# Optimization experiments

Hardware: AMD Instinct MI355X
Metric: run time of the kernel (lower is better)

## Reference

```python
import jax, jax.numpy as jnp
import numpy as np

M = 2          # n_mix
D_K = 128      # feature dim
TEMP = float(np.sqrt(D_K))  # temperature = d_k ** 0.5


def setup_inputs() -> dict:
    key = jax.random.key(0)
    k1, k2, k3, k4 = jax.random.split(key, 4)
    BS, N, N2 = 8, 2048, 2048
    qt = jax.random.normal(k1, (BS, N, D_K), jnp.float32)
    kt = jax.random.normal(k2, (BS, N2, D_K), jnp.float32)
    vt = jax.random.normal(k3, (BS, N2, D_K), jnp.float32)
    std = M ** -0.5
    kernel = jax.random.uniform(k4, (M, D_K), jnp.float32, -std, std)
    return {"qt": qt, "kt": kt, "vt": vt, "kernel": kernel}


def reference(qt, kt, vt, kernel):
    # channels_last path of MixtureOfSoftMaxACF.call, training=False (dropout = identity)
    BS, N, dk = qt.shape
    N2 = kt.shape[1]
    d = dk // M
    # mixture prior: softmax(kernel @ mean_q^T) over axis=1 (faithful to Softmax(axis=1))
    bar_qt = jnp.mean(qt, axis=1)                       # (BS, dk)
    prior_mix = jax.nn.softmax(kernel @ bar_qt.T, axis=1)  # (m, BS)
    prior_mix = prior_mix.reshape(BS * M, 1, 1)            # row-major reshape, as in TF
    # split features into mixtures via row-major reshape (as tf.reshape does)
    q = qt.reshape(BS * M, N, d)
    k = kt.reshape(BS * M, N2, d)
    att = jnp.einsum('bnd,bmd->bnm', q, k) / TEMP        # (BS*m, N, N2)
    att = jax.nn.softmax(att, axis=2)
    att = (att * prior_mix).reshape(BS, M, N, N2).sum(axis=1)  # (BS, N, N2)
    return att @ vt                                      # (BS, N, d_v)
```

## Files before the change

kernel.cpp:

```cpp
#include <hip/hip_runtime.h>
#include <hip/hip_fp16.h>

typedef float    f32x4 __attribute__((ext_vector_type(4)));
typedef _Float16 f16x2 __attribute__((ext_vector_type(2)));
typedef _Float16 f16x4 __attribute__((ext_vector_type(4)));
typedef _Float16 f16x8 __attribute__((ext_vector_type(8)));

#define BS 8
#define NN 2048
#define DK 128
#define DM 64
#define MIXOFF (1024 * DK)
#define QSCALE 0.12751744116926208f

#define MFMA32(a, b, c) __builtin_amdgcn_mfma_f32_16x16x32_f16((a), (b), (c), 0, 0, 0)
#define EXP2(x) __builtin_amdgcn_exp2f(x)

__device__ __forceinline__ f16x2 pkrtz(float x, float y) {
  return __builtin_bit_cast(f16x2, __builtin_amdgcn_cvt_pkrtz(x, y));
}

__device__ __forceinline__ void load_lds16(const _Float16* g, _Float16* l) {
  __builtin_amdgcn_global_load_lds(
      (const __attribute__((address_space(1))) void*)(uintptr_t)g,
      (__attribute__((address_space(3))) void*)(uint32_t)(uintptr_t)l, 16, 0, 0);
}

__global__ void prep_k(const float* __restrict__ kt, _Float16* __restrict__ kh,
                       const float* __restrict__ vt, _Float16* __restrict__ vT,
                       const float* __restrict__ qt, float* __restrict__ partial) {
  __shared__ float tile[64][65];
  __shared__ float red[256];
  int blk = blockIdx.x;
  int t = threadIdx.x;
  if (blk < 512) {
    size_t base = (size_t)blk * 4096;
#pragma unroll
    for (int j = 0; j < 4; ++j) {
      size_t i = base + j * 1024 + t * 4;
      f32x4 v = *(const f32x4*)(kt + i);
      f16x4 h;
      h[0] = (_Float16)v[0]; h[1] = (_Float16)v[1];
      h[2] = (_Float16)v[2]; h[3] = (_Float16)v[3];
      *(f16x4*)(kh + i) = h;
    }
  } else if (blk < 1024) {
    int i2 = blk - 512;
    int b = i2 >> 6;
    int rem = i2 & 63;
    int j0 = (rem & 31) * 64;
    int c0 = (rem >> 5) * 64;
    int tx = t & 63, ty = t >> 6;
    const float* src = vt + ((size_t)b * NN + j0) * DK + c0;
#pragma unroll
    for (int rr = 0; rr < 16; ++rr) {
      int row = ty * 16 + rr;
      tile[row][tx] = src[(size_t)row * DK + tx];
    }
    __syncthreads();
    _Float16* dst = vT + ((size_t)b * DK + c0) * NN + j0;
    int chl = t >> 4;
    int k4 = (t & 15) * 4;
#pragma unroll
    for (int r2 = 0; r2 < 4; ++r2) {
      int ch = r2 * 16 + chl;
      f16x4 h;
      h[0] = (_Float16)tile[k4 + 0][ch]; h[1] = (_Float16)tile[k4 + 1][ch];
      h[2] = (_Float16)tile[k4 + 2][ch]; h[3] = (_Float16)tile[k4 + 3][ch];
      *(f16x4*)(dst + (size_t)ch * NN + k4) = h;
    }
  } else {
    int i = blk - 1024;
    int b = i >> 3, seg = i & 7;
    int c = t & 127, h = t >> 7;
    const float* p = qt + ((size_t)b * NN + seg * 256 + h * 128) * DK + c;
    float s = 0.f;
#pragma unroll 8
    for (int n = 0; n < 128; ++n) s += p[(size_t)n * DK];
    red[t] = s;
    __syncthreads();
    if (t < 128) partial[(size_t)i * 128 + t] = red[t] + red[t + 128];
  }
}

#define STAGE(BUF, S) do {                                 \
    _Float16* db_ = stg + (BUF) * 8192;                    \
    load_lds16(khg + gKst + (S) * 2048, db_ + t * 8);      \
    load_lds16(vTg + gVst + (S) * 32, db_ + 4096 + t * 8); \
  } while (0)

__global__ __launch_bounds__(512, 2) void attn_k(const float* __restrict__ qt,
                                                 const _Float16* __restrict__ khg,
                                                 const _Float16* __restrict__ vTg,
                                                 const float* __restrict__ kern,
                                                 const float* __restrict__ partial,
                                                 float* __restrict__ out) {
  __shared__ __align__(16) char smem[40960];
  _Float16* stg = (_Float16*)smem;
  const int b = blockIdx.x & 7;
  const int qb = blockIdx.x >> 3;
  const int t = threadIdx.x;
  const int wv = t >> 6;
  const int m = wv >> 2;
  const int u = wv & 3;
  const int lane = t & 63;
  const int quad = lane >> 4, l16 = lane & 15;
  const int perm = ((l16 >> 2) << 3) | (l16 & 3);
  const int bq = b * (NN * DK);
  const int bV = b * (DK * NN);

  f16x8 qf[2];
#pragma unroll
  for (int c = 0; c < 2; ++c) {
    const float* qp_ = qt + bq + m * MIXOFF +
                       (qb * 64 + u * 16 + l16) * DM + quad * 8 + c * 32;
    f32x4 v0 = *(const f32x4*)qp_;
    f32x4 v1 = *(const f32x4*)(qp_ + 4);
    union { f16x8 v; f16x2 h[4]; } w;
    w.h[0] = pkrtz(v0[0] * QSCALE, v0[1] * QSCALE);
    w.h[1] = pkrtz(v0[2] * QSCALE, v0[3] * QSCALE);
    w.h[2] = pkrtz(v1[0] * QSCALE, v1[1] * QSCALE);
    w.h[3] = pkrtz(v1[2] * QSCALE, v1[3] * QSCALE);
    qf[c] = w.v;
  }

  const int mixu = t >> 8;
  const int qq8 = t & 255;
  const int rK = qq8 >> 3;
  const int uuK = (qq8 & 7) ^ ((rK & 3) ^ ((rK >> 3) << 1));
  const int chV = t >> 2;
  const int uuV = (t & 3) ^ ((chV + (chV >> 2)) & 3);
  const int gKst = bq + mixu * MIXOFF + rK * 64 + uuK * 8;
  const int gVst = bV + chV * NN + uuV * 8;

  const int gK = (l16 & 3) ^ ((l16 >> 2) << 1);
  const int hV = (l16 + (l16 >> 2)) & 3;
  const int kA = (quad ^ gK) * 8;
  const int kB = ((quad + 4) ^ gK) * 8;
  const int kr0 = m * 2048 + perm * 64;
  const int kr1 = m * 2048 + (perm + 4) * 64;
  const int vbase = 4096 + l16 * 32 + (quad ^ hV) * 8;

  const f32x4 z = {0.f, 0.f, 0.f, 0.f};
  f32x4 acc[8];
  float lsum = 0.f;
#pragma unroll
  for (int cc = 0; cc < 8; ++cc) acc[cc] = z;

  STAGE(0, 0);
  int buf = 0;
  for (int s = 0; s < 64; ++s) {
    __syncthreads();
    if (s + 1 < 64) STAGE(buf ^ 1, s + 1);
    const _Float16* sb_ = stg + buf * 8192;
    f16x8 kf0 = *(const f16x8*)(sb_ + kr0 + kA);
    f16x8 kf1 = *(const f16x8*)(sb_ + kr0 + kB);
    f16x8 kf2 = *(const f16x8*)(sb_ + kr1 + kA);
    f16x8 kf3 = *(const f16x8*)(sb_ + kr1 + kB);
    f32x4 s0 = MFMA32(kf1, qf[1], MFMA32(kf0, qf[0], z));
    f32x4 s1 = MFMA32(kf3, qf[1], MFMA32(kf2, qf[0], z));
    f16x8 vf[8];
#pragma unroll
    for (int cc = 0; cc < 8; ++cc) vf[cc] = *(const f16x8*)(sb_ + vbase + cc * 512);
    float e0 = EXP2(s0[0]), e1 = EXP2(s0[1]), e2 = EXP2(s0[2]), e3 = EXP2(s0[3]);
    float e4 = EXP2(s1[0]), e5 = EXP2(s1[1]), e6 = EXP2(s1[2]), e7 = EXP2(s1[3]);
    lsum += ((e0 + e1) + (e2 + e3)) + ((e4 + e5) + (e6 + e7));
    union { f16x8 v; f16x2 h[4]; } w;
    w.h[0] = pkrtz(e0, e1); w.h[1] = pkrtz(e2, e3);
    w.h[2] = pkrtz(e4, e5); w.h[3] = pkrtz(e6, e7);
#pragma unroll
    for (int cc = 0; cc < 8; ++cc) acc[cc] = MFMA32(vf[cc], w.v, acc[cc]);
    buf ^= 1;
  }
  __syncthreads();

  float* obuf = (float*)smem;
  float* barL = (float*)(smem + 33792);
  float* lgp = (float*)(smem + 37888);
  float* exq = (float*)(smem + 37952);
  float* prp = (float*)(smem + 38016);

  for (int e = t; e < 1024; e += 512) {
    int bb = e >> 7, c = e & 127;
    float ss = 0.f;
#pragma unroll
    for (int seg = 0; seg < 8; ++seg) ss += partial[(size_t)(bb * 8 + seg) * 128 + c];
    barL[e] = ss * (1.0f / 2048.0f);
  }
  __syncthreads();
  if (t < 16) {
    int mm = t >> 3, bb = t & 7;
    float ss = 0.f;
    for (int c = 0; c < DK; ++c) ss += kern[mm * DK + c] * barL[bb * 128 + c];
    lgp[t] = ss;
  }
  __syncthreads();
  if (t < 16) {
    int mm = t >> 3;
    float mx = lgp[mm * 8];
    for (int i = 1; i < 8; ++i) mx = fmaxf(mx, lgp[mm * 8 + i]);
    exq[t] = __expf(lgp[t] - mx);
  }
  __syncthreads();
  if (t < 16) {
    int mm = t >> 3;
    float sm = 0.f;
    for (int i = 0; i < 8; ++i) sm += exq[mm * 8 + i];
    prp[t] = exq[t] / sm;
  }
  __syncthreads();

  lsum += __shfl_xor(lsum, 16);
  lsum += __shfl_xor(lsum, 32);
  const float r_ = prp[b * 2 + m] / lsum;

  const int orow = (u * 16 + l16) * 132;
  if (m == 0) {
#pragma unroll
    for (int cc = 0; cc < 8; ++cc) {
      f32x4 o;
#pragma unroll
      for (int e = 0; e < 4; ++e) o[e] = acc[cc][e] * r_;
      *(f32x4*)&obuf[orow + cc * 16 + quad * 4] = o;
    }
  }
  __syncthreads();
  if (m == 1) {
#pragma unroll
    for (int cc = 0; cc < 8; ++cc) {
      f32x4 o = *(const f32x4*)&obuf[orow + cc * 16 + quad * 4];
#pragma unroll
      for (int e = 0; e < 4; ++e) o[e] += acc[cc][e] * r_;
      *(f32x4*)&obuf[orow + cc * 16 + quad * 4] = o;
    }
  }
  __syncthreads();
  const int row = t >> 3;
  const int cb = (t & 7) * 16;
  float* op = out + ((size_t)b * NN + qb * 64 + row) * DK + cb;
#pragma unroll
  for (int g = 0; g < 4; ++g)
    *(f32x4*)(op + g * 4) = *(const f32x4*)&obuf[row * 132 + cb + g * 4];
}

extern "C" void kernel_launch(void* const* d_in, const int* in_sizes, int n_in,
                              void* d_out, int out_size, void* d_ws, size_t ws_size,
                              hipStream_t stream) {
  const float* qt = (const float*)d_in[0];
  const float* kt = (const float*)d_in[1];
  const float* vt = (const float*)d_in[2];
  const float* kern = (const float*)d_in[3];
  float* out = (float*)d_out;

  char* ws = (char*)d_ws;
  float* partial = (float*)ws;
  _Float16* khp = (_Float16*)(ws + 65536);
  _Float16* vTp = khp + (size_t)BS * NN * DK;

  prep_k<<<dim3(1088), dim3(256), 0, stream>>>(kt, khp, vt, vTp, qt, partial);
  attn_k<<<dim3(256), dim3(512), 0, stream>>>(qt, khp, vTp, kern, partial, out);
}
```

Measured before the change: 118.2 us.

## Split key range across block pairs and double query rows per wave

Each block now covers 128 query rows (two 16-row sub-tiles per wave) but only half of the key sequence. Each staged K/V tile therefore feeds twice as many MFMAs, halving LDS traffic per useful FLOP. The two halves write unnormalised accumulators and row sums to a global workspace slot. An atomic counter picks the second-arriving block to merge both halves, normalise and write the output. This adds workspace traffic, an extra memset launch, a threadfence/atomic handshake and higher register pressure from doubled accumulators.

```diff
diff --git a/kernel.cpp b/kernel.cpp
--- a/kernel.cpp
+++ b/kernel.cpp
@@ -12,6 +12,7 @@
 #define DM 64
 #define MIXOFF (1024 * DK)
 #define QSCALE 0.12751744116926208f
+#define SLOTF 33024
 
 #define MFMA32(a, b, c) __builtin_amdgcn_mfma_f32_16x16x32_f16((a), (b), (c), 0, 0, 0)
 #define EXP2(x) __builtin_amdgcn_exp2f(x)
@@ -28,7 +29,7 @@
 
 __global__ void prep_k(const float* __restrict__ kt, _Float16* __restrict__ kh,
                        const float* __restrict__ vt, _Float16* __restrict__ vT,
-                       const float* __restrict__ qt, float* __restrict__ partial) {
+                       const float* __restrict__ qt, float* __restrict__ qpart) {
   __shared__ float tile[64][65];
   __shared__ float red[256];
   int blk = blockIdx.x;
@@ -79,7 +80,7 @@
     for (int n = 0; n < 128; ++n) s += p[(size_t)n * DK];
     red[t] = s;
     __syncthreads();
-    if (t < 128) partial[(size_t)i * 128 + t] = red[t] + red[t + 128];
+    if (t < 128) qpart[(size_t)i * 128 + t] = red[t] + red[t + 128];
   }
 }
 
@@ -93,12 +94,16 @@
                                                  const _Float16* __restrict__ khg,
                                                  const _Float16* __restrict__ vTg,
                                                  const float* __restrict__ kern,
-                                                 const float* __restrict__ partial,
+                                                 const float* __restrict__ qpart,
+                                                 float* __restrict__ slots,
+                                                 int* __restrict__ counters,
                                                  float* __restrict__ out) {
   __shared__ __align__(16) char smem[40960];
   _Float16* stg = (_Float16*)smem;
   const int b = blockIdx.x & 7;
-  const int qb = blockIdx.x >> 3;
+  const int qb = (blockIdx.x >> 3) & 15;
+  const int kh = blockIdx.x >> 7;
+  const int pair = blockIdx.x & 127;
   const int t = threadIdx.x;
   const int wv = t >> 6;
   const int m = wv >> 2;
@@ -109,20 +114,22 @@
   const int bq = b * (NN * DK);
   const int bV = b * (DK * NN);
 
-  f16x8 qf[2];
-#pragma unroll
-  for (int c = 0; c < 2; ++c) {
-    const float* qp_ = qt + bq + m * MIXOFF +
-                       (qb * 64 + u * 16 + l16) * DM + quad * 8 + c * 32;
-    f32x4 v0 = *(const f32x4*)qp_;
-    f32x4 v1 = *(const f32x4*)(qp_ + 4);
-    union { f16x8 v; f16x2 h[4]; } w;
-    w.h[0] = pkrtz(v0[0] * QSCALE, v0[1] * QSCALE);
-    w.h[1] = pkrtz(v0[2] * QSCALE, v0[3] * QSCALE);
-    w.h[2] = pkrtz(v1[0] * QSCALE, v1[1] * QSCALE);
-    w.h[3] = pkrtz(v1[2] * QSCALE, v1[3] * QSCALE);
-    qf[c] = w.v;
-  }
+  f16x8 qf[2][2];
+#pragma unroll
+  for (int su = 0; su < 2; ++su)
+#pragma unroll
+    for (int c = 0; c < 2; ++c) {
+      const float* qp_ = qt + bq + m * MIXOFF +
+                         (qb * 128 + u * 32 + su * 16 + l16) * DM + quad * 8 + c * 32;
+      f32x4 v0 = *(const f32x4*)qp_;
+      f32x4 v1 = *(const f32x4*)(qp_ + 4);
+      union { f16x8 v; f16x2 h[4]; } w;
+      w.h[0] = pkrtz(v0[0] * QSCALE, v0[1] * QSCALE);
+      w.h[1] = pkrtz(v0[2] * QSCALE, v0[3] * QSCALE);
+      w.h[2] = pkrtz(v1[0] * QSCALE, v1[1] * QSCALE);
+      w.h[3] = pkrtz(v1[2] * QSCALE, v1[3] * QSCALE);
+      qf[su][c] = w.v;
+    }
 
   const int mixu = t >> 8;
   const int qq8 = t & 255;
@@ -130,8 +137,8 @@
   const int uuK = (qq8 & 7) ^ ((rK & 3) ^ ((rK >> 3) << 1));
   const int chV = t >> 2;
   const int uuV = (t & 3) ^ ((chV + (chV >> 2)) & 3);
-  const int gKst = bq + mixu * MIXOFF + rK * 64 + uuK * 8;
-  const int gVst = bV + chV * NN + uuV * 8;
+  const int gKst = bq + mixu * MIXOFF + kh * (1024 * DM) + rK * 64 + uuK * 8;
+  const int gVst = bV + chV * NN + kh * 1024 + uuV * 8;
 
   const int gK = (l16 & 3) ^ ((l16 >> 2) << 1);
   const int hV = (l16 + (l16 >> 2)) & 3;
@@ -142,49 +149,74 @@
   const int vbase = 4096 + l16 * 32 + (quad ^ hV) * 8;
 
   const f32x4 z = {0.f, 0.f, 0.f, 0.f};
-  f32x4 acc[8];
-  float lsum = 0.f;
-#pragma unroll
-  for (int cc = 0; cc < 8; ++cc) acc[cc] = z;
+  f32x4 acc[2][8];
+  float lsum[2] = {0.f, 0.f};
+#pragma unroll
+  for (int su = 0; su < 2; ++su)
+#pragma unroll
+    for (int cc = 0; cc < 8; ++cc) acc[su][cc] = z;
 
   STAGE(0, 0);
   int buf = 0;
-  for (int s = 0; s < 64; ++s) {
-    __syncthreads();
-    if (s + 1 < 64) STAGE(buf ^ 1, s + 1);
+  for (int s = 0; s < 32; ++s) {
+    __syncthreads();
+    if (s + 1 < 32) STAGE(buf ^ 1, s + 1);
     const _Float16* sb_ = stg + buf * 8192;
     f16x8 kf0 = *(const f16x8*)(sb_ + kr0 + kA);
     f16x8 kf1 = *(const f16x8*)(sb_ + kr0 + kB);
     f16x8 kf2 = *(const f16x8*)(sb_ + kr1 + kA);
     f16x8 kf3 = *(const f16x8*)(sb_ + kr1 + kB);
-    f32x4 s0 = MFMA32(kf1, qf[1], MFMA32(kf0, qf[0], z));
-    f32x4 s1 = MFMA32(kf3, qf[1], MFMA32(kf2, qf[0], z));
     f16x8 vf[8];
 #pragma unroll
     for (int cc = 0; cc < 8; ++cc) vf[cc] = *(const f16x8*)(sb_ + vbase + cc * 512);
-    float e0 = EXP2(s0[0]), e1 = EXP2(s0[1]), e2 = EXP2(s0[2]), e3 = EXP2(s0[3]);
-    float e4 = EXP2(s1[0]), e5 = EXP2(s1[1]), e6 = EXP2(s1[2]), e7 = EXP2(s1[3]);
-    lsum += ((e0 + e1) + (e2 + e3)) + ((e4 + e5) + (e6 + e7));
-    union { f16x8 v; f16x2 h[4]; } w;
-    w.h[0] = pkrtz(e0, e1); w.h[1] = pkrtz(e2, e3);
-    w.h[2] = pkrtz(e4, e5); w.h[3] = pkrtz(e6, e7);
-#pragma unroll
-    for (int cc = 0; cc < 8; ++cc) acc[cc] = MFMA32(vf[cc], w.v, acc[cc]);
+#pragma unroll
+    for (int su = 0; su < 2; ++su) {
+      f32x4 s0 = MFMA32(kf1, qf[su][1], MFMA32(kf0, qf[su][0], z));
+      f32x4 s1 = MFMA32(kf3, qf[su][1], MFMA32(kf2, qf[su][0], z));
+      float e0 = EXP2(s0[0]), e1 = EXP2(s0[1]), e2 = EXP2(s0[2]), e3 = EXP2(s0[3]);
+      float e4 = EXP2(s1[0]), e5 = EXP2(s1[1]), e6 = EXP2(s1[2]), e7 = EXP2(s1[3]);
+      lsum[su] += ((e0 + e1) + (e2 + e3)) + ((e4 + e5) + (e6 + e7));
+      union { f16x8 v; f16x2 h[4]; } w;
+      w.h[0] = pkrtz(e0, e1); w.h[1] = pkrtz(e2, e3);
+      w.h[2] = pkrtz(e4, e5); w.h[3] = pkrtz(e6, e7);
+#pragma unroll
+      for (int cc = 0; cc < 8; ++cc) acc[su][cc] = MFMA32(vf[cc], w.v, acc[su][cc]);
+    }
     buf ^= 1;
   }
-  __syncthreads();
+
+#pragma unroll
+  for (int su = 0; su < 2; ++su) {
+    lsum[su] += __shfl_xor(lsum[su], 16);
+    lsum[su] += __shfl_xor(lsum[su], 32);
+  }
+
+  float* slot = slots + (size_t)pair * (2 * SLOTF) + (size_t)kh * SLOTF;
+#pragma unroll
+  for (int su = 0; su < 2; ++su) {
+    int r_ = (m * 128 + u * 32 + su * 16 + l16) * 128 + quad * 4;
+#pragma unroll
+    for (int cc = 0; cc < 8; ++cc)
+      *(f32x4*)(slot + r_ + cc * 16) = acc[su][cc];
+    if (quad == 0) slot[32768 + m * 128 + u * 32 + su * 16 + l16] = lsum[su];
+  }
+  __threadfence();
+  int* flagp = (int*)(smem + 38912);
+  if (t == 0) *flagp = atomicAdd(&counters[pair], 1);
+  __syncthreads();
+  if (*flagp == 0) return;
+  __threadfence();
 
   float* obuf = (float*)smem;
   float* barL = (float*)(smem + 33792);
   float* lgp = (float*)(smem + 37888);
   float* exq = (float*)(smem + 37952);
   float* prp = (float*)(smem + 38016);
-
   for (int e = t; e < 1024; e += 512) {
     int bb = e >> 7, c = e & 127;
     float ss = 0.f;
 #pragma unroll
-    for (int seg = 0; seg < 8; ++seg) ss += partial[(size_t)(bb * 8 + seg) * 128 + c];
+    for (int seg = 0; seg < 8; ++seg) ss += qpart[(size_t)(bb * 8 + seg) * 128 + c];
     barL[e] = ss * (1.0f / 2048.0f);
   }
   __syncthreads();
@@ -210,37 +242,59 @@
   }
   __syncthreads();
 
-  lsum += __shfl_xor(lsum, 16);
-  lsum += __shfl_xor(lsum, 32);
-  const float r_ = prp[b * 2 + m] / lsum;
-
-  const int orow = (u * 16 + l16) * 132;
-  if (m == 0) {
+  const float* pslot = slots + (size_t)pair * (2 * SLOTF) + (size_t)(kh ^ 1) * SLOTF;
+  float rr[2];
+#pragma unroll
+  for (int su = 0; su < 2; ++su) {
+    int r_ = (m * 128 + u * 32 + su * 16 + l16) * 128 + quad * 4;
 #pragma unroll
     for (int cc = 0; cc < 8; ++cc) {
-      f32x4 o;
-#pragma unroll
-      for (int e = 0; e < 4; ++e) o[e] = acc[cc][e] * r_;
-      *(f32x4*)&obuf[orow + cc * 16 + quad * 4] = o;
-    }
-  }
-  __syncthreads();
-  if (m == 1) {
-#pragma unroll
-    for (int cc = 0; cc < 8; ++cc) {
-      f32x4 o = *(const f32x4*)&obuf[orow + cc * 16 + quad * 4];
-#pragma unroll
-      for (int e = 0; e < 4; ++e) o[e] += acc[cc][e] * r_;
-      *(f32x4*)&obuf[orow + cc * 16 + quad * 4] = o;
-    }
-  }
-  __syncthreads();
-  const int row = t >> 3;
-  const int cb = (t & 7) * 16;
-  float* op = out + ((size_t)b * NN + qb * 64 + row) * DK + cb;
-#pragma unroll
-  for (int g = 0; g < 4; ++g)
-    *(f32x4*)(op + g * 4) = *(const f32x4*)&obuf[row * 132 + cb + g * 4];
+      f32x4 po = *(const f32x4*)(pslot + r_ + cc * 16);
+#pragma unroll
+      for (int e = 0; e < 4; ++e) acc[su][cc][e] += po[e];
+    }
+    float pl = pslot[32768 + m * 128 + u * 32 + su * 16 + l16];
+    rr[su] = prp[b * 2 + m] / (lsum[su] + pl);
+  }
+
+#pragma unroll
+  for (int p = 0; p < 2; ++p) {
+    __syncthreads();
+    if ((u >> 1) == p && m == 0) {
+#pragma unroll
+      for (int su = 0; su < 2; ++su) {
+        int r_ = ((u & 1) * 32 + su * 16 + l16) * 132 + quad * 4;
+#pragma unroll
+        for (int cc = 0; cc < 8; ++cc) {
+          f32x4 o;
+#pragma unroll
+          for (int e = 0; e < 4; ++e) o[e] = acc[su][cc][e] * rr[su];
+          *(f32x4*)&obuf[r_ + cc * 16] = o;
+        }
+      }
+    }
+    __syncthreads();
+    if ((u >> 1) == p && m == 1) {
+#pragma unroll
+      for (int su = 0; su < 2; ++su) {
+        int r_ = ((u & 1) * 32 + su * 16 + l16) * 132 + quad * 4;
+#pragma unroll
+        for (int cc = 0; cc < 8; ++cc) {
+          f32x4 o = *(const f32x4*)&obuf[r_ + cc * 16];
+#pragma unroll
+          for (int e = 0; e < 4; ++e) o[e] += acc[su][cc][e] * rr[su];
+          *(f32x4*)&obuf[r_ + cc * 16] = o;
+        }
+      }
+    }
+    __syncthreads();
+    const int row = t >> 3;
+    const int cb = (t & 7) * 16;
+    float* op = out + ((size_t)b * NN + qb * 128 + p * 64 + row) * DK + cb;
+#pragma unroll
+    for (int g = 0; g < 4; ++g)
+      *(f32x4*)(op + g * 4) = *(const f32x4*)&obuf[row * 132 + cb + g * 4];
+  }
 }
 
 extern "C" void kernel_launch(void* const* d_in, const int* in_sizes, int n_in,
@@ -253,10 +307,14 @@
   float* out = (float*)d_out;
 
   char* ws = (char*)d_ws;
-  float* partial = (float*)ws;
+  int* counters = (int*)ws;
+  float* qpart = (float*)(ws + 4096);
   _Float16* khp = (_Float16*)(ws + 65536);
   _Float16* vTp = khp + (size_t)BS * NN * DK;
-
-  prep_k<<<dim3(1088), dim3(256), 0, stream>>>(kt, khp, vt, vTp, qt, partial);
-  attn_k<<<dim3(256), dim3(512), 0, stream>>>(qt, khp, vTp, kern, partial, out);
-}
+  float* slots = (float*)(ws + (16u << 20));
+
+  hipMemsetAsync(counters, 0, 512, stream);
+  prep_k<<<dim3(1088), dim3(256), 0, stream>>>(kt, khp, vt, vTp, qt, qpart);
+  attn_k<<<dim3(256), dim3(512), 0, stream>>>(qt, khp, vTp, kern, qpart, slots,
+                                              counters, out);
+}
```

Result: slower. 189.9 us (+60.7%).
